# Performance work log

Measured on AMD Instinct MI355X. Metric: run time of the kernel, lower is better.

Reference implementation:

```python
import jax, jax.numpy as jnp
from jax import lax
import numpy as np

STYLE_STRENGTH = 1.0
PATCH = 3
TOL = 1e-14


def covsqrt_mean(feature, inverse=False):
    # feature: [b, c, h, w]; matches torch covsqrt_mean with eigenvalue truncation.
    b, c, h, w = feature.shape
    f = feature.reshape(b, c, h * w)
    mean = jnp.mean(f, axis=2, keepdims=True)
    zm = f - mean
    cov = jnp.einsum('bcn,bdn->bcd', zm, zm)  # unnormalized covariance, [b,c,c]
    evals, evecs = jnp.linalg.eigh(cov)       # ascending evals, like torch
    p = -0.5 if inverse else 0.5
    # torch keeps evals[k:] where k is the first index with eval > tol; since
    # evals are sorted ascending this equals masking evals > tol.
    mask = evals > TOL
    d = jnp.where(mask, jnp.where(mask, evals, 1.0) ** p, 0.0)
    covsqrt = jnp.einsum('bij,bj,bkj->bik', evecs, d, evecs)
    return covsqrt, mean


def whitening(feature):
    b, c, h, w = feature.shape
    inv_cs, mean = covsqrt_mean(feature, inverse=True)
    out = jnp.einsum('bcd,bdn->bcn', inv_cs, feature.reshape(b, c, -1) - mean)
    return out.reshape(b, c, h, w)


def coloring(feature, target):
    b, c, h, w = feature.shape
    cs, mean = covsqrt_mean(target, inverse=False)
    out = jnp.einsum('bcd,bdn->bcn', cs, feature.reshape(b, c, -1)) + mean
    return out.reshape(b, c, h, w)


def extract_kernels(feat, k):
    # feat [b,c,h,w] -> per-location style patches as conv kernels [b, h*w, c, k, k]
    b, c, h, w = feat.shape
    pad = (k - 1) // 2
    fp = jnp.pad(feat, ((0, 0), (0, 0), (pad, pad), (pad, pad)))
    # stack the k*k shifted views: [b, c, h, w, k*k] in (ky, kx) row-major order,
    # matching torch unfold(2,k).unfold(3,k) flattening.
    patches = jnp.stack([fp[:, :, dy:dy + h, dx:dx + w]
                         for dy in range(k) for dx in range(k)], axis=-1)
    return patches.reshape(b, c, h * w, k * k).transpose(0, 2, 1, 3).reshape(b, h * w, c, k, k)


def reassemble(norm_c, norm_s, k):
    b, c, h, w = norm_c.shape
    ker = extract_kernels(norm_s, k)                                  # [b, hw_s, c, k, k]
    knorm = jnp.sqrt(jnp.sum(ker ** 2, axis=(2, 3, 4), keepdims=True))
    pad = (k - 1) // 2

    def conv_one(feat, kk):
        # feat [c,h,w], kk [hw_s,c,k,k] -> score [hw_s,h,w]
        x = jnp.pad(feat, ((0, 0), (pad, pad), (pad, pad)))[None]
        return lax.conv_general_dilated(x, kk, (1, 1), 'VALID')[0]

    score = jax.vmap(conv_one)(norm_c, ker / knorm)                   # [b, hw_s, h, w]
    idx = jnp.argmax(score, axis=1)                                   # [b, h, w]
    onehot = jax.nn.one_hot(idx, score.shape[1], dtype=score.dtype).transpose(0, 3, 1, 2)

    def deconv_one(oh, kk):
        # conv_transpose2d(padded onehot, kk, padding=k-1) == VALID conv with
        # spatially flipped kernel (in/out channels swapped).
        x = jnp.pad(oh, ((0, 0), (pad, pad), (pad, pad)))[None]        # [1, hw_s, h+2p, w+2p]
        wf = jnp.flip(kk, axis=(2, 3)).transpose(1, 0, 2, 3)           # [c, hw_s, k, k]
        return lax.conv_general_dilated(x, wf, (1, 1), 'VALID')[0]     # [c, h, w]

    out = jax.vmap(deconv_one)(onehot, ker)                           # [b, c, h, w]
    # overlap-count normalization: separable box filter of ones
    cnt_h = jnp.convolve(jnp.ones(h, out.dtype), jnp.ones(k, out.dtype), mode='same')
    cnt_w = jnp.convolve(jnp.ones(w, out.dtype), jnp.ones(k, out.dtype), mode='same')
    deconv_norm = (cnt_h[:, None] * cnt_w[None, :])[None, None]
    return out / deconv_norm


def setup_inputs() -> dict:
    key = jax.random.key(0)
    k1, k2 = jax.random.split(key)
    b, ch, h, w = 2, 256, 48, 48
    c = jax.random.normal(k1, (b, ch, h, w), dtype=jnp.float32)
    s = jax.random.normal(k2, (b, ch, h, w), dtype=jnp.float32)
    return {'c': c, 's': s}


def reference(c, s):
    norm_c = whitening(c)
    norm_s = whitening(s)
    rF = reassemble(norm_c, norm_s, PATCH)
    sF = coloring(rF, s)
    return (1.0 - STYLE_STRENGTH) * c + STYLE_STRENGTH * sF
```

## Files before the change

kernel.cpp:

```cpp
#include <hip/hip_runtime.h>
#include <math.h>

#define HW 2304
#define NC 256
#define NPIX 2500
#define NPIXP 2560
#define MATSZ 65536
#define NS_ITERS 5
#define NSLAB 6
#define KSLAB 384
#define PMSZ (2560 * 256)

typedef unsigned long long u64;
typedef unsigned short ushortt;
typedef __attribute__((ext_vector_type(8))) short bhalf8;
typedef __attribute__((ext_vector_type(4))) float f32x4;

__global__ void mean_kernel(const float* __restrict__ c, const float* __restrict__ s,
                            double* __restrict__ mean) {
  int ch = blockIdx.x, m = blockIdx.y;
  const float* src = (m < 2 ? c + m * (NC * HW) : s + (m - 2) * (NC * HW)) + ch * HW;
  double acc = 0.0;
  for (int n = threadIdx.x; n < HW; n += 64) acc += (double)src[n];
  for (int o = 32; o > 0; o >>= 1) acc += __shfl_down(acc, o);
  if (threadIdx.x == 0) mean[m * NC + ch] = acc / (double)HW;
}

__launch_bounds__(256)
__global__ void cov_part(const float* __restrict__ c, const float* __restrict__ s,
                         float* __restrict__ covp) {
  int z = blockIdx.z;
  int m = z / NSLAB, slab = z % NSLAB;
  const float* src = (m < 2 ? c + m * (NC * HW) : s + (m - 2) * (NC * HW));
  int i0 = blockIdx.y * 64, j0 = blockIdx.x * 64;
  int kb = slab * KSLAB;
  __shared__ float As[16][64], Bs[16][64];
  int tx = threadIdx.x, ty = threadIdx.y;
  int tid = ty * 16 + tx;
  int li = tid >> 2;
  int lk4 = tid & 3;
  float acc[4][4] = {};
  for (int kc = 0; kc < KSLAB; kc += 16) {
    __syncthreads();
    float4 va = *(const float4*)&src[(u64)(i0 + li) * HW + kb + kc + lk4 * 4];
    float4 vb = *(const float4*)&src[(u64)(j0 + li) * HW + kb + kc + lk4 * 4];
    As[lk4 * 4 + 0][li] = va.x; As[lk4 * 4 + 1][li] = va.y;
    As[lk4 * 4 + 2][li] = va.z; As[lk4 * 4 + 3][li] = va.w;
    Bs[lk4 * 4 + 0][li] = vb.x; Bs[lk4 * 4 + 1][li] = vb.y;
    Bs[lk4 * 4 + 2][li] = vb.z; Bs[lk4 * 4 + 3][li] = vb.w;
    __syncthreads();
    #pragma unroll
    for (int kk = 0; kk < 16; ++kk) {
      float4 a = *(const float4*)&As[kk][ty * 4];
      float4 b = *(const float4*)&Bs[kk][tx * 4];
      float av[4] = {a.x, a.y, a.z, a.w};
      float bv[4] = {b.x, b.y, b.z, b.w};
      #pragma unroll
      for (int i = 0; i < 4; ++i)
        #pragma unroll
        for (int j = 0; j < 4; ++j) acc[i][j] += av[i] * bv[j];
    }
  }
  float* Cp = covp + (u64)z * MATSZ;
  #pragma unroll
  for (int i = 0; i < 4; ++i) {
    float4 v = make_float4(acc[i][0], acc[i][1], acc[i][2], acc[i][3]);
    *(float4*)&Cp[(i0 + ty * 4 + i) * NC + j0 + tx * 4] = v;
  }
}

__global__ void cov_reduce(const float* __restrict__ covp, const double* __restrict__ mean,
                           float* __restrict__ cov, double* __restrict__ snorm) {
  int m = blockIdx.y;
  int row = blockIdx.x, col = threadIdx.x;
  int e = row * 256 + col;
  float v = 0.0f;
  #pragma unroll
  for (int slab = 0; slab < NSLAB; ++slab)
    v += covp[(u64)(m * NSLAB + slab) * MATSZ + e];
  double mi = mean[m * NC + row], mj = mean[m * NC + col];
  float res = (float)((double)v - (double)HW * mi * mj);
  cov[m * MATSZ + e] = res;
  if (col == row) atomicAdd(&snorm[m], 1.25 * (double)res / 256.0);
}

__global__ void ns_init(const float* __restrict__ cov, const double* __restrict__ snorm,
                        float* __restrict__ Y, float* __restrict__ Z) {
  int m = blockIdx.y;
  int e = blockIdx.x * 256 + threadIdx.x;
  double inv = 1.0 / snorm[m];
  Y[m * MATSZ + e] = (float)((double)cov[m * MATSZ + e] * inv);
  Z[m * MATSZ + e] = ((e >> 8) == (e & 255)) ? 1.0f : 0.0f;
}

__launch_bounds__(256)
__global__ void ns_gemm_T(const float* __restrict__ Zc, const float* __restrict__ Yc,
                          float* __restrict__ T) {
  int m = blockIdx.z;
  const float* A = Zc + m * MATSZ;
  const float* B = Yc + m * MATSZ;
  int m0 = blockIdx.y * 32, n0 = blockIdx.x * 32;
  __shared__ float As[32][33], Bs[32][33];
  int tx = threadIdx.x, ty = threadIdx.y;
  int tid = ty * 16 + tx;
  float acc[2][2] = {};
  for (int k0 = 0; k0 < 256; k0 += 32) {
    __syncthreads();
    #pragma unroll
    for (int l = 0; l < 4; ++l) {
      int idx = tid + l * 256;
      int r = idx >> 5, cc = idx & 31;
      As[r][cc] = A[(m0 + r) * NC + k0 + cc];
      Bs[r][cc] = B[(k0 + r) * NC + n0 + cc];
    }
    __syncthreads();
    #pragma unroll
    for (int kk = 0; kk < 32; ++kk) {
      float a0 = As[ty][kk], a1 = As[ty + 16][kk];
      float b0 = Bs[kk][tx], b1 = Bs[kk][tx + 16];
      acc[0][0] += a0 * b0; acc[0][1] += a0 * b1;
      acc[1][0] += a1 * b0; acc[1][1] += a1 * b1;
    }
  }
  float* Cp = T + m * MATSZ;
  #pragma unroll
  for (int i = 0; i < 2; ++i)
    #pragma unroll
    for (int j = 0; j < 2; ++j) {
      int row = m0 + ty + 16 * i, col = n0 + tx + 16 * j;
      Cp[row * NC + col] = (row == col ? 1.5f : 0.0f) - 0.5f * acc[i][j];
    }
}

__launch_bounds__(256)
__global__ void ns_gemm_YZ(const float* __restrict__ Yc, const float* __restrict__ Zc,
                           const float* __restrict__ T,
                           float* __restrict__ Yn, float* __restrict__ Zn) {
  int z = blockIdx.z;
  int m = z & 3;
  bool isY = (z < 4);
  const float* A = isY ? (Yc + m * MATSZ) : (T + m * MATSZ);
  const float* B = isY ? (T + m * MATSZ) : (Zc + m * MATSZ);
  float* Cp = isY ? (Yn + m * MATSZ) : (Zn + m * MATSZ);
  int m0 = blockIdx.y * 32, n0 = blockIdx.x * 32;
  __shared__ float As[32][33], Bs[32][33];
  int tx = threadIdx.x, ty = threadIdx.y;
  int tid = ty * 16 + tx;
  float acc[2][2] = {};
  for (int k0 = 0; k0 < 256; k0 += 32) {
    __syncthreads();
    #pragma unroll
    for (int l = 0; l < 4; ++l) {
      int idx = tid + l * 256;
      int r = idx >> 5, cc = idx & 31;
      As[r][cc] = A[(m0 + r) * NC + k0 + cc];
      Bs[r][cc] = B[(k0 + r) * NC + n0 + cc];
    }
    __syncthreads();
    #pragma unroll
    for (int kk = 0; kk < 32; ++kk) {
      float a0 = As[ty][kk], a1 = As[ty + 16][kk];
      float b0 = Bs[kk][tx], b1 = Bs[kk][tx + 16];
      acc[0][0] += a0 * b0; acc[0][1] += a0 * b1;
      acc[1][0] += a1 * b0; acc[1][1] += a1 * b1;
    }
  }
  #pragma unroll
  for (int i = 0; i < 2; ++i)
    #pragma unroll
    for (int j = 0; j < 2; ++j)
      Cp[(m0 + ty + 16 * i) * NC + n0 + tx + 16 * j] = acc[i][j];
}

__launch_bounds__(256)
__global__ void whiten_kernel(const float* __restrict__ c, const float* __restrict__ s,
                              const float* __restrict__ Zf,
                              const double* __restrict__ snorm, const double* __restrict__ mean,
                              float* __restrict__ padC_cf, float* __restrict__ padS_cf,
                              float* __restrict__ padS_cl) {
  int mat = blockIdx.z;
  const float* src = (mat < 2 ? c + mat * (NC * HW) : s + (mat - 2) * (NC * HW));
  const float* A = Zf + mat * MATSZ;
  const double* mn = mean + mat * NC;
  float wscale = (float)(1.0 / sqrt(snorm[mat]));
  int m0 = blockIdx.y * 64, n0 = blockIdx.x * 64;
  __shared__ float As[16][68], Bs[16][68];
  int tid = threadIdx.x;
  int tx = tid & 15, ty = tid >> 4;
  int li = tid >> 2, lk4 = tid & 3;
  int kr = tid >> 4, p4 = (tid & 15) * 4;
  float acc[4][4] = {};
  for (int kc = 0; kc < 256; kc += 16) {
    __syncthreads();
    float4 va = *(const float4*)&A[(u64)(m0 + li) * NC + kc + lk4 * 4];
    As[lk4 * 4 + 0][li] = va.x; As[lk4 * 4 + 1][li] = va.y;
    As[lk4 * 4 + 2][li] = va.z; As[lk4 * 4 + 3][li] = va.w;
    float mk = (float)mn[kc + kr];
    float4 vb = *(const float4*)&src[(u64)(kc + kr) * HW + n0 + p4];
    vb.x -= mk; vb.y -= mk; vb.z -= mk; vb.w -= mk;
    *(float4*)&Bs[kr][p4] = vb;
    __syncthreads();
    #pragma unroll
    for (int kk = 0; kk < 16; ++kk) {
      float4 a = *(const float4*)&As[kk][ty * 4];
      float4 b = *(const float4*)&Bs[kk][tx * 4];
      float av[4] = {a.x, a.y, a.z, a.w};
      float bv[4] = {b.x, b.y, b.z, b.w};
      #pragma unroll
      for (int i = 0; i < 4; ++i)
        #pragma unroll
        for (int j = 0; j < 4; ++j) acc[i][j] += av[i] * bv[j];
    }
  }
  #pragma unroll
  for (int i = 0; i < 4; ++i) {
    int row = m0 + ty * 4 + i;
    #pragma unroll
    for (int j = 0; j < 4; ++j) {
      int n = n0 + tx * 4 + j;
      float v = acc[i][j] * wscale;
      int y = n / 48, x = n % 48;
      int ppos = (y + 1) * 50 + (x + 1);
      if (mat < 2) {
        padC_cf[(u64)mat * (NC * NPIXP) + row * NPIXP + ppos] = v;
      } else {
        padS_cf[(u64)(mat - 2) * (NC * NPIXP) + row * NPIXP + ppos] = v;
        padS_cl[(u64)(mat - 2) * (NPIX * NC) + ppos * NC + row] = v;
      }
    }
  }
}

__launch_bounds__(256)
__global__ void tsplit_kernel(const float* __restrict__ padC_cf, const float* __restrict__ padS_cf,
                              ushortt* __restrict__ padCk_hi, ushortt* __restrict__ padCk_lo,
                              ushortt* __restrict__ padSk_hi, ushortt* __restrict__ padSk_lo) {
  int p0 = blockIdx.x * 64;
  int by = blockIdx.y;
  const float* src = (by < 2) ? padC_cf + (u64)by * (NC * NPIXP)
                              : padS_cf + (u64)(by - 2) * (NC * NPIXP);
  ushortt* dhi = (by < 2) ? padCk_hi + (u64)by * PMSZ : padSk_hi + (u64)(by - 2) * PMSZ;
  ushortt* dlo = (by < 2) ? padCk_lo + (u64)by * PMSZ : padSk_lo + (u64)(by - 2) * PMSZ;
  __shared__ float Tk[64][68];
  int tid = threadIdx.x;
  int rr = tid >> 4, c4 = (tid & 15) * 4;
  int p = tid >> 2, kg = (tid & 3) * 16;
  for (int ks = 0; ks < 256; ks += 64) {
    __syncthreads();
    #pragma unroll
    for (int it = 0; it < 4; ++it) {
      int r = rr + it * 16;
      *(float4*)&Tk[r][c4] = *(const float4*)&src[(u64)(ks + r) * NPIXP + p0 + c4];
    }
    __syncthreads();
    __align__(16) ushortt h[16], lo[16];
    #pragma unroll
    for (int e = 0; e < 16; ++e) {
      float v = Tk[kg + e][p];
      unsigned bb = __float_as_uint(v);
      unsigned hu = (bb + 0x7FFFu + ((bb >> 16) & 1u)) >> 16;
      float hf = __uint_as_float(hu << 16);
      float rres = v - hf;
      unsigned lb = __float_as_uint(rres);
      unsigned lu = (lb + 0x7FFFu + ((lb >> 16) & 1u)) >> 16;
      h[e] = (ushortt)hu;
      lo[e] = (ushortt)lu;
    }
    u64 off = (u64)(p0 + p) * 256 + ks + kg;
    *(uint4*)&dhi[off] = *(const uint4*)&h[0];
    *(uint4*)&dhi[off + 8] = *(const uint4*)&h[8];
    *(uint4*)&dlo[off] = *(const uint4*)&lo[0];
    *(uint4*)&dlo[off + 8] = *(const uint4*)&lo[8];
  }
}

__global__ void knorm_kernel(const float* __restrict__ padS_cl, float* __restrict__ rknorm) {
  int ps = blockIdx.x, b = blockIdx.y;
  int ys = ps / 48, xs = ps % 48;
  const float* S = padS_cl + (u64)b * (NPIX * NC);
  int ch = threadIdx.x;
  double acc = 0.0;
  #pragma unroll
  for (int dy = 0; dy < 3; ++dy)
    #pragma unroll
    for (int dx = 0; dx < 3; ++dx) {
      float v = S[((ys + dy) * 50 + xs + dx) * NC + ch];
      acc += (double)v * (double)v;
    }
  __shared__ double sd[256];
  int t = threadIdx.x;
  sd[t] = acc; __syncthreads();
  for (int st = 128; st > 0; st >>= 1) {
    if (t < st) sd[t] += sd[t + st];
    __syncthreads();
  }
  if (ch == 0) rknorm[b * HW + ps] = (float)(1.0 / sqrt(sd[0]));
}

__launch_bounds__(256)
__global__ void gram_mfma(const ushortt* __restrict__ Ah_g, const ushortt* __restrict__ Al_g,
                          const ushortt* __restrict__ Bh_g, const ushortt* __restrict__ Bl_g,
                          float* __restrict__ G) {
  __shared__ ushortt As_hi[128 * 32], As_lo[128 * 32], Bs_hi[64 * 32], Bs_lo[64 * 32];
  int tid = threadIdx.x;
  int wv = tid >> 6, l = tid & 63, lr = l & 15, lk = l >> 4;
  int p0 = blockIdx.x * 128, q0 = blockIdx.y * 64;
  int arow = tid >> 2;
  int apart = (tid & 3) * 8;
  const ushortt* pAh0 = Ah_g + (u64)(p0 + arow) * 256 + apart;
  const ushortt* pAh1 = Ah_g + (u64)(p0 + arow + 64) * 256 + apart;
  const ushortt* pAl0 = Al_g + (u64)(p0 + arow) * 256 + apart;
  const ushortt* pAl1 = Al_g + (u64)(p0 + arow + 64) * 256 + apart;
  const ushortt* pBh  = Bh_g + (u64)(q0 + arow) * 256 + apart;
  const ushortt* pBl  = Bl_g + (u64)(q0 + arow) * 256 + apart;
  float4 rAh0 = *(const float4*)pAh0;
  float4 rAh1 = *(const float4*)pAh1;
  float4 rAl0 = *(const float4*)pAl0;
  float4 rAl1 = *(const float4*)pAl1;
  float4 rBh  = *(const float4*)pBh;
  float4 rBl  = *(const float4*)pBl;
  f32x4 acc[2][4];
  #pragma unroll
  for (int a = 0; a < 2; ++a)
    #pragma unroll
    for (int b = 0; b < 4; ++b)
      #pragma unroll
      for (int e = 0; e < 4; ++e) acc[a][b][e] = 0.0f;
  for (int k0 = 0; k0 < 256; k0 += 32) {
    __syncthreads();
    *(float4*)&As_hi[arow * 32 + apart] = rAh0;
    *(float4*)&As_hi[(arow + 64) * 32 + apart] = rAh1;
    *(float4*)&As_lo[arow * 32 + apart] = rAl0;
    *(float4*)&As_lo[(arow + 64) * 32 + apart] = rAl1;
    *(float4*)&Bs_hi[arow * 32 + apart] = rBh;
    *(float4*)&Bs_lo[arow * 32 + apart] = rBl;
    __syncthreads();
    if (k0 + 32 < 256) {
      rAh0 = *(const float4*)(pAh0 + k0 + 32);
      rAh1 = *(const float4*)(pAh1 + k0 + 32);
      rAl0 = *(const float4*)(pAl0 + k0 + 32);
      rAl1 = *(const float4*)(pAl1 + k0 + 32);
      rBh  = *(const float4*)(pBh + k0 + 32);
      rBl  = *(const float4*)(pBl + k0 + 32);
    }
    bhalf8 Ah[2], Al[2], Bh[4], Bl[4];
    #pragma unroll
    for (int a = 0; a < 2; ++a) {
      int off = (wv * 32 + a * 16 + lr) * 32 + lk * 8;
      Ah[a] = *(const bhalf8*)&As_hi[off];
      Al[a] = *(const bhalf8*)&As_lo[off];
    }
    #pragma unroll
    for (int b = 0; b < 4; ++b) {
      int off = (b * 16 + lr) * 32 + lk * 8;
      Bh[b] = *(const bhalf8*)&Bs_hi[off];
      Bl[b] = *(const bhalf8*)&Bs_lo[off];
    }
    #pragma unroll
    for (int a = 0; a < 2; ++a)
      #pragma unroll
      for (int b = 0; b < 4; ++b) {
        acc[a][b] = __builtin_amdgcn_mfma_f32_16x16x32_bf16(Ah[a], Bh[b], acc[a][b], 0, 0, 0);
        acc[a][b] = __builtin_amdgcn_mfma_f32_16x16x32_bf16(Ah[a], Bl[b], acc[a][b], 0, 0, 0);
        acc[a][b] = __builtin_amdgcn_mfma_f32_16x16x32_bf16(Al[a], Bh[b], acc[a][b], 0, 0, 0);
      }
  }
  #pragma unroll
  for (int a = 0; a < 2; ++a)
    #pragma unroll
    for (int b = 0; b < 4; ++b)
      #pragma unroll
      for (int r = 0; r < 4; ++r) {
        int p = p0 + wv * 32 + a * 16 + lk * 4 + r;
        int q = q0 + b * 16 + lr;
        G[(u64)p * NPIXP + q] = acc[a][b][r];
      }
}

__launch_bounds__(256)
__global__ void scoremax_kernel(const float* __restrict__ G, const float* __restrict__ rknorm,
                                u64* __restrict__ rmax, int b) {
  int y = blockIdx.x, ys = blockIdx.y;
  __shared__ float Gt[3][50][50];
  __shared__ float sc[48][48];
  __shared__ float rkl[48];
  int tid = threadIdx.x;
  for (int t = tid; t < 7500; t += 256) {
    int dy = t / 2500, rem = t % 2500;
    int u = rem / 50, v = rem - u * 50;
    Gt[dy][u][v] = G[(u64)((y + dy) * 50 + u) * NPIXP + (ys + dy) * 50 + v];
  }
  if (tid < 48) rkl[tid] = rknorm[b * HW + ys * 48 + tid];
  __syncthreads();
  #pragma unroll
  for (int k = 0; k < 9; ++k) {
    int idx = tid + k * 256;
    int x = idx / 48, xs = idx - x * 48;
    float v = 0.0f;
    #pragma unroll
    for (int dy = 0; dy < 3; ++dy)
      #pragma unroll
      for (int dx = 0; dx < 3; ++dx)
        v += Gt[dy][x + dx][xs + dx];
    sc[x][xs] = v * rkl[xs];
  }
  __syncthreads();
  if (tid < 48) {
    float best = -1e30f; int bxs = 0;
    for (int xs = 0; xs < 48; ++xs) {
      float v = sc[tid][xs];
      if (v > best) { best = v; bxs = xs; }
    }
    int ps = ys * 48 + bxs;
    unsigned ub = __float_as_uint(best);
    unsigned enc = (ub & 0x80000000u) ? ~ub : (ub | 0x80000000u);
    u64 key = ((u64)enc << 32) | (u64)(2303 - ps);
    atomicMax(&rmax[(u64)b * HW + y * 48 + tid], key);
  }
}

__global__ void reassemble_kernel(const float* __restrict__ padS_cl, const u64* __restrict__ rmax,
                                  float* __restrict__ rF_cl) {
  int pix = blockIdx.x, b = blockIdx.y;
  int y = pix / 48, x = pix % 48;
  const u64* rm = rmax + (u64)b * HW;
  const float* S = padS_cl + (u64)b * (NPIX * NC);
  int ch = threadIdx.x;
  float sum = 0.0f;
  #pragma unroll
  for (int i = 0; i < 3; ++i)
    #pragma unroll
    for (int j = 0; j < 3; ++j) {
      int yn = y + 1 - i, xn = x + 1 - j;
      if (yn >= 0 && yn < 48 && xn >= 0 && xn < 48) {
        int ps = 2303 - (int)(unsigned)(rm[yn * 48 + xn] & 0xFFFFFFFFu);
        int ys = ps / 48, xs = ps % 48;
        sum += S[((ys + i) * 50 + xs + j) * NC + ch];
      }
    }
  float cy = (y == 0 || y == 47) ? 2.0f : 3.0f;
  float cx = (x == 0 || x == 47) ? 2.0f : 3.0f;
  rF_cl[(u64)b * (HW * NC) + pix * NC + ch] = sum / (cy * cx);
}

__launch_bounds__(256)
__global__ void coloring_kernel(const float* __restrict__ Yf, const double* __restrict__ snorm,
                                const double* __restrict__ mean, const float* __restrict__ rF_cl,
                                float* __restrict__ out) {
  int b = blockIdx.z;
  const float* A = Yf + (2 + b) * MATSZ;
  const float* Bp = rF_cl + (u64)b * (HW * NC);
  const double* mn = mean + (2 + b) * NC;
  float cscale = (float)sqrt(snorm[2 + b]);
  int m0 = blockIdx.y * 64, n0 = blockIdx.x * 64;
  __shared__ float As[16][68], Bs[16][68];
  int tid = threadIdx.x;
  int tx = tid & 15, ty = tid >> 4;
  int li = tid >> 2, lk4 = tid & 3;
  int pix = tid >> 2, kq = (tid & 3) * 4;
  float acc[4][4] = {};
  for (int kc = 0; kc < 256; kc += 16) {
    __syncthreads();
    float4 va = *(const float4*)&A[(u64)(m0 + li) * NC + kc + lk4 * 4];
    As[lk4 * 4 + 0][li] = va.x; As[lk4 * 4 + 1][li] = va.y;
    As[lk4 * 4 + 2][li] = va.z; As[lk4 * 4 + 3][li] = va.w;
    float4 vb = *(const float4*)&Bp[(u64)(n0 + pix) * NC + kc + kq];
    Bs[kq + 0][pix] = vb.x; Bs[kq + 1][pix] = vb.y;
    Bs[kq + 2][pix] = vb.z; Bs[kq + 3][pix] = vb.w;
    __syncthreads();
    #pragma unroll
    for (int kk = 0; kk < 16; ++kk) {
      float4 a = *(const float4*)&As[kk][ty * 4];
      float4 b2 = *(const float4*)&Bs[kk][tx * 4];
      float av[4] = {a.x, a.y, a.z, a.w};
      float bv[4] = {b2.x, b2.y, b2.z, b2.w};
      #pragma unroll
      for (int i = 0; i < 4; ++i)
        #pragma unroll
        for (int j = 0; j < 4; ++j) acc[i][j] += av[i] * bv[j];
    }
  }
  #pragma unroll
  for (int i = 0; i < 4; ++i) {
    int row = m0 + ty * 4 + i;
    float madd = (float)mn[row];
    float4 v = make_float4(acc[i][0] * cscale + madd, acc[i][1] * cscale + madd,
                           acc[i][2] * cscale + madd, acc[i][3] * cscale + madd);
    *(float4*)&out[(u64)b * (NC * HW) + (u64)row * HW + n0 + tx * 4] = v;
  }
}

extern "C" void kernel_launch(void* const* d_in, const int* in_sizes, int n_in,
                              void* d_out, int out_size, void* d_ws, size_t ws_size,
                              hipStream_t stream) {
  const float* c = (const float*)d_in[0];
  const float* s = (const float*)d_in[1];
  float* out = (float*)d_out;

  char* ws = (char*)d_ws;
  size_t off = 0;
  auto alloc = [&](size_t bytes) {
    void* p = ws + off;
    off = (off + bytes + 255) & ~(size_t)255;
    return p;
  };
  double* mean   = (double*)alloc(4 * NC * sizeof(double));
  float* cov     = (float*)alloc((size_t)4 * MATSZ * sizeof(float));
  float* covp    = (float*)alloc((size_t)4 * NSLAB * MATSZ * sizeof(float));
  float* Ya      = (float*)alloc((size_t)4 * MATSZ * sizeof(float));
  float* Yb      = (float*)alloc((size_t)4 * MATSZ * sizeof(float));
  float* Za      = (float*)alloc((size_t)4 * MATSZ * sizeof(float));
  float* Zb      = (float*)alloc((size_t)4 * MATSZ * sizeof(float));
  float* T       = (float*)alloc((size_t)4 * MATSZ * sizeof(float));
  float* padC_cf = (float*)alloc((size_t)2 * NC * NPIXP * sizeof(float));
  float* padS_cf = (float*)alloc((size_t)2 * NC * NPIXP * sizeof(float));
  float* padS_cl = (float*)alloc((size_t)2 * NPIX * NC * sizeof(float));
  ushortt* padCk_hi = (ushortt*)alloc((size_t)2 * PMSZ * sizeof(ushortt));
  ushortt* padCk_lo = (ushortt*)alloc((size_t)2 * PMSZ * sizeof(ushortt));
  ushortt* padSk_hi = (ushortt*)alloc((size_t)2 * PMSZ * sizeof(ushortt));
  ushortt* padSk_lo = (ushortt*)alloc((size_t)2 * PMSZ * sizeof(ushortt));
  float* rknorm  = (float*)alloc((size_t)2 * HW * sizeof(float));
  float* rF_cl   = (float*)alloc((size_t)2 * HW * NC * sizeof(float));
  float* G       = (float*)alloc((size_t)NPIXP * NPIXP * sizeof(float));
  u64*   rmax    = (u64*)alloc((size_t)2 * HW * sizeof(u64));
  double* snorm  = (double*)alloc(4 * sizeof(double));

  size_t padBytes = (size_t)(2 * NC * NPIXP + 2 * NC * NPIXP + 2 * NPIX * NC) * sizeof(float);
  hipMemsetAsync(padC_cf, 0, padBytes, stream);
  hipMemsetAsync(rmax, 0, (size_t)2 * HW * sizeof(u64) + 4 * sizeof(double), stream);

  mean_kernel<<<dim3(256, 4), 64, 0, stream>>>(c, s, mean);
  cov_part<<<dim3(4, 4, 4 * NSLAB), dim3(16, 16), 0, stream>>>(c, s, covp);
  cov_reduce<<<dim3(256, 4), 256, 0, stream>>>(covp, mean, cov, snorm);
  ns_init<<<dim3(256, 4), 256, 0, stream>>>(cov, snorm, Ya, Za);

  float *Yc = Ya, *Zc = Za, *Yn = Yb, *Zn = Zb;
  for (int it = 0; it < NS_ITERS; ++it) {
    ns_gemm_T<<<dim3(8, 8, 4), dim3(16, 16), 0, stream>>>(Zc, Yc, T);
    ns_gemm_YZ<<<dim3(8, 8, 8), dim3(16, 16), 0, stream>>>(Yc, Zc, T, Yn, Zn);
    float* t1 = Yc; Yc = Yn; Yn = t1;
    float* t2 = Zc; Zc = Zn; Zn = t2;
  }

  whiten_kernel<<<dim3(36, 4, 4), 256, 0, stream>>>(c, s, Zc, snorm, mean,
                                                    padC_cf, padS_cf, padS_cl);
  tsplit_kernel<<<dim3(40, 4), 256, 0, stream>>>(padC_cf, padS_cf,
                                                 padCk_hi, padCk_lo, padSk_hi, padSk_lo);
  knorm_kernel<<<dim3(2304, 2), 256, 0, stream>>>(padS_cl, rknorm);

  for (int b = 0; b < 2; ++b) {
    gram_mfma<<<dim3(20, 40), 256, 0, stream>>>(padCk_hi + (u64)b * PMSZ,
                                                padCk_lo + (u64)b * PMSZ,
                                                padSk_hi + (u64)b * PMSZ,
                                                padSk_lo + (u64)b * PMSZ, G);
    scoremax_kernel<<<dim3(48, 48), 256, 0, stream>>>(G, rknorm, rmax, b);
  }

  reassemble_kernel<<<dim3(2304, 2), 256, 0, stream>>>(padS_cl, rmax, rF_cl);
  coloring_kernel<<<dim3(36, 4, 2), 256, 0, stream>>>(Yc, snorm, mean, rF_cl, out);
}
```

Before: 359.7 us.

## Fuse setup kernels, specialize first Newton-Schulz step, batch gram and scoremax

Computes the trace normalizer in the mean kernel and folds ns_init into cov_reduce, which now writes Y0 and Z1 = 1.5I - 0.5Y0 directly. The first Newton-Schulz iteration therefore needs only a single GEMM (Y1 = Y0·Z1), since Z0 is the identity. Removes knorm_kernel by having tsplit emit per-pixel squared norms that scoremax sums over the 3x3 window. Gram and scoremax are launched once over both batches using a doubled G buffer. This cuts launches and redundant work, at the cost of float rather than double precision in the norm accumulation and more workspace memory.

```diff
diff --git a/kernel.cpp b/kernel.cpp
--- a/kernel.cpp
+++ b/kernel.cpp
@@ -10,6 +10,7 @@
 #define NSLAB 6
 #define KSLAB 384
 #define PMSZ (2560 * 256)
+#define GSZ ((u64)NPIXP * NPIXP)
 
 typedef unsigned long long u64;
 typedef unsigned short ushortt;
@@ -17,13 +18,23 @@
 typedef __attribute__((ext_vector_type(4))) float f32x4;
 
 __global__ void mean_kernel(const float* __restrict__ c, const float* __restrict__ s,
-                            double* __restrict__ mean) {
+                            double* __restrict__ mean, double* __restrict__ snorm) {
   int ch = blockIdx.x, m = blockIdx.y;
   const float* src = (m < 2 ? c + m * (NC * HW) : s + (m - 2) * (NC * HW)) + ch * HW;
-  double acc = 0.0;
-  for (int n = threadIdx.x; n < HW; n += 64) acc += (double)src[n];
-  for (int o = 32; o > 0; o >>= 1) acc += __shfl_down(acc, o);
-  if (threadIdx.x == 0) mean[m * NC + ch] = acc / (double)HW;
+  double acc = 0.0, acc2 = 0.0;
+  for (int n = threadIdx.x; n < HW; n += 64) {
+    double v = (double)src[n];
+    acc += v; acc2 += v * v;
+  }
+  for (int o = 32; o > 0; o >>= 1) {
+    acc += __shfl_down(acc, o);
+    acc2 += __shfl_down(acc2, o);
+  }
+  if (threadIdx.x == 0) {
+    mean[m * NC + ch] = acc / (double)HW;
+    double diag = acc2 - acc * acc / (double)HW;
+    atomicAdd(&snorm[m], 1.25 * diag / 256.0);
+  }
 }
 
 __launch_bounds__(256)
@@ -70,7 +81,8 @@
 }
 
 __global__ void cov_reduce(const float* __restrict__ covp, const double* __restrict__ mean,
-                           float* __restrict__ cov, double* __restrict__ snorm) {
+                           const double* __restrict__ snorm,
+                           float* __restrict__ Y0, float* __restrict__ Z1) {
   int m = blockIdx.y;
   int row = blockIdx.x, col = threadIdx.x;
   int e = row * 256 + col;
@@ -80,17 +92,47 @@
     v += covp[(u64)(m * NSLAB + slab) * MATSZ + e];
   double mi = mean[m * NC + row], mj = mean[m * NC + col];
   float res = (float)((double)v - (double)HW * mi * mj);
-  cov[m * MATSZ + e] = res;
-  if (col == row) atomicAdd(&snorm[m], 1.25 * (double)res / 256.0);
-}
-
-__global__ void ns_init(const float* __restrict__ cov, const double* __restrict__ snorm,
-                        float* __restrict__ Y, float* __restrict__ Z) {
-  int m = blockIdx.y;
-  int e = blockIdx.x * 256 + threadIdx.x;
-  double inv = 1.0 / snorm[m];
-  Y[m * MATSZ + e] = (float)((double)cov[m * MATSZ + e] * inv);
-  Z[m * MATSZ + e] = ((e >> 8) == (e & 255)) ? 1.0f : 0.0f;
+  float inv = (float)(1.0 / snorm[m]);
+  float y0 = res * inv;
+  Y0[m * MATSZ + e] = y0;
+  Z1[m * MATSZ + e] = ((row == col) ? 1.5f : 0.0f) - 0.5f * y0;
+}
+
+__launch_bounds__(256)
+__global__ void ns_gemm_Y(const float* __restrict__ Y0, const float* __restrict__ T0,
+                          float* __restrict__ Y1) {
+  int m = blockIdx.z;
+  const float* A = Y0 + m * MATSZ;
+  const float* B = T0 + m * MATSZ;
+  float* Cp = Y1 + m * MATSZ;
+  int m0 = blockIdx.y * 32, n0 = blockIdx.x * 32;
+  __shared__ float As[32][33], Bs[32][33];
+  int tx = threadIdx.x, ty = threadIdx.y;
+  int tid = ty * 16 + tx;
+  float acc[2][2] = {};
+  for (int k0 = 0; k0 < 256; k0 += 32) {
+    __syncthreads();
+    #pragma unroll
+    for (int l = 0; l < 4; ++l) {
+      int idx = tid + l * 256;
+      int r = idx >> 5, cc = idx & 31;
+      As[r][cc] = A[(m0 + r) * NC + k0 + cc];
+      Bs[r][cc] = B[(k0 + r) * NC + n0 + cc];
+    }
+    __syncthreads();
+    #pragma unroll
+    for (int kk = 0; kk < 32; ++kk) {
+      float a0 = As[ty][kk], a1 = As[ty + 16][kk];
+      float b0 = Bs[kk][tx], b1 = Bs[kk][tx + 16];
+      acc[0][0] += a0 * b0; acc[0][1] += a0 * b1;
+      acc[1][0] += a1 * b0; acc[1][1] += a1 * b1;
+    }
+  }
+  #pragma unroll
+  for (int i = 0; i < 2; ++i)
+    #pragma unroll
+    for (int j = 0; j < 2; ++j)
+      Cp[(m0 + ty + 16 * i) * NC + n0 + tx + 16 * j] = acc[i][j];
 }
 
 __launch_bounds__(256)
@@ -234,7 +276,8 @@
 __launch_bounds__(256)
 __global__ void tsplit_kernel(const float* __restrict__ padC_cf, const float* __restrict__ padS_cf,
                               ushortt* __restrict__ padCk_hi, ushortt* __restrict__ padCk_lo,
-                              ushortt* __restrict__ padSk_hi, ushortt* __restrict__ padSk_lo) {
+                              ushortt* __restrict__ padSk_hi, ushortt* __restrict__ padSk_lo,
+                              float* __restrict__ ssq) {
   int p0 = blockIdx.x * 64;
   int by = blockIdx.y;
   const float* src = (by < 2) ? padC_cf + (u64)by * (NC * NPIXP)
@@ -245,6 +288,7 @@
   int tid = threadIdx.x;
   int rr = tid >> 4, c4 = (tid & 15) * 4;
   int p = tid >> 2, kg = (tid & 3) * 16;
+  float sq = 0.0f;
   for (int ks = 0; ks < 256; ks += 64) {
     __syncthreads();
     #pragma unroll
@@ -257,6 +301,7 @@
     #pragma unroll
     for (int e = 0; e < 16; ++e) {
       float v = Tk[kg + e][p];
+      sq += v * v;
       unsigned bb = __float_as_uint(v);
       unsigned hu = (bb + 0x7FFFu + ((bb >> 16) & 1u)) >> 16;
       float hf = __uint_as_float(hu << 16);
@@ -272,35 +317,22 @@
     *(uint4*)&dlo[off] = *(const uint4*)&lo[0];
     *(uint4*)&dlo[off + 8] = *(const uint4*)&lo[8];
   }
-}
-
-__global__ void knorm_kernel(const float* __restrict__ padS_cl, float* __restrict__ rknorm) {
-  int ps = blockIdx.x, b = blockIdx.y;
-  int ys = ps / 48, xs = ps % 48;
-  const float* S = padS_cl + (u64)b * (NPIX * NC);
-  int ch = threadIdx.x;
-  double acc = 0.0;
-  #pragma unroll
-  for (int dy = 0; dy < 3; ++dy)
-    #pragma unroll
-    for (int dx = 0; dx < 3; ++dx) {
-      float v = S[((ys + dy) * 50 + xs + dx) * NC + ch];
-      acc += (double)v * (double)v;
-    }
-  __shared__ double sd[256];
-  int t = threadIdx.x;
-  sd[t] = acc; __syncthreads();
-  for (int st = 128; st > 0; st >>= 1) {
-    if (t < st) sd[t] += sd[t + st];
-    __syncthreads();
-  }
-  if (ch == 0) rknorm[b * HW + ps] = (float)(1.0 / sqrt(sd[0]));
-}
-
-__launch_bounds__(256)
-__global__ void gram_mfma(const ushortt* __restrict__ Ah_g, const ushortt* __restrict__ Al_g,
-                          const ushortt* __restrict__ Bh_g, const ushortt* __restrict__ Bl_g,
-                          float* __restrict__ G) {
+  sq += __shfl_down(sq, 2);
+  sq += __shfl_down(sq, 1);
+  if (by >= 2 && (tid & 3) == 0 && (p0 + p) < NPIX)
+    ssq[(u64)(by - 2) * NPIX + p0 + p] = sq;
+}
+
+__launch_bounds__(256)
+__global__ void gram_mfma(const ushortt* __restrict__ Ah_b, const ushortt* __restrict__ Al_b,
+                          const ushortt* __restrict__ Bh_b, const ushortt* __restrict__ Bl_b,
+                          float* __restrict__ Gb) {
+  int bz = blockIdx.z;
+  const ushortt* Ah_g = Ah_b + (u64)bz * PMSZ;
+  const ushortt* Al_g = Al_b + (u64)bz * PMSZ;
+  const ushortt* Bh_g = Bh_b + (u64)bz * PMSZ;
+  const ushortt* Bl_g = Bl_b + (u64)bz * PMSZ;
+  float* G = Gb + (u64)bz * GSZ;
   __shared__ ushortt As_hi[128 * 32], As_lo[128 * 32], Bs_hi[64 * 32], Bs_lo[64 * 32];
   int tid = threadIdx.x;
   int wv = tid >> 6, l = tid & 63, lr = l & 15, lk = l >> 4;
@@ -378,11 +410,14 @@
 }
 
 __launch_bounds__(256)
-__global__ void scoremax_kernel(const float* __restrict__ G, const float* __restrict__ rknorm,
-                                u64* __restrict__ rmax, int b) {
-  int y = blockIdx.x, ys = blockIdx.y;
+__global__ void scoremax_kernel(const float* __restrict__ Gb, const float* __restrict__ ssq,
+                                u64* __restrict__ rmax) {
+  int y = blockIdx.x, ys = blockIdx.y, b = blockIdx.z;
+  const float* G = Gb + (u64)b * GSZ;
+  const float* sq = ssq + (u64)b * NPIX;
   __shared__ float Gt[3][50][50];
   __shared__ float sc[48][48];
+  __shared__ float sr[152];
   __shared__ float rkl[48];
   int tid = threadIdx.x;
   for (int t = tid; t < 7500; t += 256) {
@@ -390,7 +425,19 @@
     int u = rem / 50, v = rem - u * 50;
     Gt[dy][u][v] = G[(u64)((y + dy) * 50 + u) * NPIXP + (ys + dy) * 50 + v];
   }
-  if (tid < 48) rkl[tid] = rknorm[b * HW + ys * 48 + tid];
+  if (tid < 150) {
+    int dy = tid / 50, v = tid - dy * 50;
+    sr[dy * 50 + v] = sq[(ys + dy) * 50 + v];
+  }
+  __syncthreads();
+  if (tid < 48) {
+    float t = 0.0f;
+    #pragma unroll
+    for (int dy = 0; dy < 3; ++dy)
+      #pragma unroll
+      for (int dx = 0; dx < 3; ++dx) t += sr[dy * 50 + tid + dx];
+    rkl[tid] = 1.0f / sqrtf(t);
+  }
   __syncthreads();
   #pragma unroll
   for (int k = 0; k < 9; ++k) {
@@ -505,7 +552,6 @@
     return p;
   };
   double* mean   = (double*)alloc(4 * NC * sizeof(double));
-  float* cov     = (float*)alloc((size_t)4 * MATSZ * sizeof(float));
   float* covp    = (float*)alloc((size_t)4 * NSLAB * MATSZ * sizeof(float));
   float* Ya      = (float*)alloc((size_t)4 * MATSZ * sizeof(float));
   float* Yb      = (float*)alloc((size_t)4 * MATSZ * sizeof(float));
@@ -519,9 +565,9 @@
   ushortt* padCk_lo = (ushortt*)alloc((size_t)2 * PMSZ * sizeof(ushortt));
   ushortt* padSk_hi = (ushortt*)alloc((size_t)2 * PMSZ * sizeof(ushortt));
   ushortt* padSk_lo = (ushortt*)alloc((size_t)2 * PMSZ * sizeof(ushortt));
-  float* rknorm  = (float*)alloc((size_t)2 * HW * sizeof(float));
+  float* ssq     = (float*)alloc((size_t)2 * NPIX * sizeof(float));
   float* rF_cl   = (float*)alloc((size_t)2 * HW * NC * sizeof(float));
-  float* G       = (float*)alloc((size_t)NPIXP * NPIXP * sizeof(float));
+  float* G       = (float*)alloc((size_t)2 * GSZ * sizeof(float));
   u64*   rmax    = (u64*)alloc((size_t)2 * HW * sizeof(u64));
   double* snorm  = (double*)alloc(4 * sizeof(double));
 
@@ -529,13 +575,13 @@
   hipMemsetAsync(padC_cf, 0, padBytes, stream);
   hipMemsetAsync(rmax, 0, (size_t)2 * HW * sizeof(u64) + 4 * sizeof(double), stream);
 
-  mean_kernel<<<dim3(256, 4), 64, 0, stream>>>(c, s, mean);
+  mean_kernel<<<dim3(256, 4), 64, 0, stream>>>(c, s, mean, snorm);
   cov_part<<<dim3(4, 4, 4 * NSLAB), dim3(16, 16), 0, stream>>>(c, s, covp);
-  cov_reduce<<<dim3(256, 4), 256, 0, stream>>>(covp, mean, cov, snorm);
-  ns_init<<<dim3(256, 4), 256, 0, stream>>>(cov, snorm, Ya, Za);
-
-  float *Yc = Ya, *Zc = Za, *Yn = Yb, *Zn = Zb;
-  for (int it = 0; it < NS_ITERS; ++it) {
+  cov_reduce<<<dim3(256, 4), 256, 0, stream>>>(covp, mean, snorm, Ya, Za);
+  ns_gemm_Y<<<dim3(8, 8, 4), dim3(16, 16), 0, stream>>>(Ya, Za, Yb);
+
+  float *Yc = Yb, *Zc = Za, *Yn = Ya, *Zn = Zb;
+  for (int it = 1; it < NS_ITERS; ++it) {
     ns_gemm_T<<<dim3(8, 8, 4), dim3(16, 16), 0, stream>>>(Zc, Yc, T);
     ns_gemm_YZ<<<dim3(8, 8, 8), dim3(16, 16), 0, stream>>>(Yc, Zc, T, Yn, Zn);
     float* t1 = Yc; Yc = Yn; Yn = t1;
@@ -545,16 +591,10 @@
   whiten_kernel<<<dim3(36, 4, 4), 256, 0, stream>>>(c, s, Zc, snorm, mean,
                                                     padC_cf, padS_cf, padS_cl);
   tsplit_kernel<<<dim3(40, 4), 256, 0, stream>>>(padC_cf, padS_cf,
-                                                 padCk_hi, padCk_lo, padSk_hi, padSk_lo);
-  knorm_kernel<<<dim3(2304, 2), 256, 0, stream>>>(padS_cl, rknorm);
-
-  for (int b = 0; b < 2; ++b) {
-    gram_mfma<<<dim3(20, 40), 256, 0, stream>>>(padCk_hi + (u64)b * PMSZ,
-                                                padCk_lo + (u64)b * PMSZ,
-                                                padSk_hi + (u64)b * PMSZ,
-                                                padSk_lo + (u64)b * PMSZ, G);
-    scoremax_kernel<<<dim3(48, 48), 256, 0, stream>>>(G, rknorm, rmax, b);
-  }
+                                                 padCk_hi, padCk_lo, padSk_hi, padSk_lo, ssq);
+
+  gram_mfma<<<dim3(20, 40, 2), 256, 0, stream>>>(padCk_hi, padCk_lo, padSk_hi, padSk_lo, G);
+  scoremax_kernel<<<dim3(48, 48, 2), 256, 0, stream>>>(G, ssq, rmax);
 
   reassemble_kernel<<<dim3(2304, 2), 256, 0, stream>>>(padS_cl, rmax, rF_cl);
   coloring_kernel<<<dim3(36, 4, 2), 256, 0, stream>>>(Yc, snorm, mean, rF_cl, out);
```

Result: faster. 322.1 us (-10.4%).
